# Optimization experiments

Hardware: AMD Instinct MI355X
Metric: run time of the kernel (lower is better)

The kernel has to match this reference:

```python
import jax, jax.numpy as jnp
import numpy as np

N, E, IN_DIM, HID, G, NCLS, LAYERS = 200000, 1200000, 128, 64, 1024, 6, 3
BN_EPS = 1e-5


def _bn(x, g, b, m, v):
    # eval-mode BatchNorm1d with running stats
    return (x - m) * jax.lax.rsqrt(v + BN_EPS) * g + b


def setup_inputs() -> dict:
    key = jax.random.key(0)
    ks = jax.random.split(key, 24)
    s = 0.05
    d = {
        "x": jax.random.normal(ks[0], (N, IN_DIM), jnp.float32),
        "edge_index": jax.random.randint(ks[1], (2, E), 0, N, dtype=jnp.int32),
        "batch": jnp.sort(jax.random.randint(ks[2], (N,), 0, G, dtype=jnp.int32)),
        # input embedding + input BN
        "emb_w": jax.random.normal(ks[3], (IN_DIM, HID), jnp.float32) * s,
        "emb_b": jnp.zeros((HID,), jnp.float32),
        "ibn_g": jnp.ones((HID,), jnp.float32),
        "ibn_b": jnp.zeros((HID,), jnp.float32),
        "ibn_m": jax.random.normal(ks[4], (HID,), jnp.float32) * 0.1,
        "ibn_v": jax.random.uniform(ks[5], (HID,), jnp.float32, 0.5, 1.5),
        # stacked per-layer GIN MLP params [LAYERS, ...]
        "fc1_w": jax.random.normal(ks[6], (LAYERS, HID, HID), jnp.float32) * s,
        "fc1_b": jnp.zeros((LAYERS, HID), jnp.float32),
        "mbn_g": jnp.ones((LAYERS, HID), jnp.float32),
        "mbn_b": jnp.zeros((LAYERS, HID), jnp.float32),
        "mbn_m": jax.random.normal(ks[7], (LAYERS, HID), jnp.float32) * 0.1,
        "mbn_v": jax.random.uniform(ks[8], (LAYERS, HID), jnp.float32, 0.5, 1.5),
        "fc2_w": jax.random.normal(ks[9], (LAYERS, HID, HID), jnp.float32) * s,
        "fc2_b": jnp.zeros((LAYERS, HID), jnp.float32),
        # stacked per-layer outer BN params
        "obn_g": jnp.ones((LAYERS, HID), jnp.float32),
        "obn_b": jnp.zeros((LAYERS, HID), jnp.float32),
        "obn_m": jax.random.normal(ks[10], (LAYERS, HID), jnp.float32) * 0.1,
        "obn_v": jax.random.uniform(ks[11], (LAYERS, HID), jnp.float32, 0.5, 1.5),
        # classifier head
        "cls1_w": jax.random.normal(ks[12], (HID, HID // 2), jnp.float32) * s,
        "cls1_b": jnp.zeros((HID // 2,), jnp.float32),
        "cls2_w": jax.random.normal(ks[13], (HID // 2, NCLS), jnp.float32) * s,
        "cls2_b": jnp.zeros((NCLS,), jnp.float32),
    }
    return d


def reference(x, edge_index, batch,
              emb_w, emb_b, ibn_g, ibn_b, ibn_m, ibn_v,
              fc1_w, fc1_b, mbn_g, mbn_b, mbn_m, mbn_v, fc2_w, fc2_b,
              obn_g, obn_b, obn_m, obn_v,
              cls1_w, cls1_b, cls2_w, cls2_b):
    n = x.shape[0]
    src, dst = edge_index[0], edge_index[1]

    # input embed -> BN -> relu (dropout = identity in eval)
    h = jnp.dot(x, emb_w) + emb_b
    h = jax.nn.relu(_bn(h, ibn_g, ibn_b, ibn_m, ibn_v))

    for i in range(LAYERS):
        # GINConv (eps=0): aggregate neighbors via scatter-add, then MLP
        agg = jax.ops.segment_sum(h[src], dst, num_segments=n)
        z = h + agg
        z = jnp.dot(z, fc1_w[i]) + fc1_b[i]
        z = jax.nn.relu(_bn(z, mbn_g[i], mbn_b[i], mbn_m[i], mbn_v[i]))
        z = jnp.dot(z, fc2_w[i]) + fc2_b[i]
        # outer BN + relu
        h = jax.nn.relu(_bn(z, obn_g[i], obn_b[i], obn_m[i], obn_v[i]))

    # global mean pool per graph
    sums = jax.ops.segment_sum(h, batch, num_segments=G)
    cnts = jax.ops.segment_sum(jnp.ones((n,), h.dtype), batch, num_segments=G)
    pooled = sums / jnp.maximum(cnts, 1.0)[:, None]

    # classifier
    out = jax.nn.relu(jnp.dot(pooled, cls1_w) + cls1_b)
    out = jnp.dot(out, cls2_w) + cls2_b
    return out
```

## Files before the change

kernel.cpp:

```cpp
#include <hip/hip_runtime.h>
#include <hip/hip_bf16.h>

#define N_NODES 200000
#define N_EDGES 1200000
#define IN_DIM  128
#define HID     64
#define NGRAPH  1024
#define NCLS    6
#define BN_EPS  1e-5f

#define TILE_N   64
#define ZS       68
#define ECAP     1024

#define NBKT   128
#define BRANGE 1568
#define BCAP   12288
#define EPB    4096
#define NB_BIN ((N_EDGES + EPB - 1) / EPB)

#define SWZ(s) ((s) ^ (((s) >> 4) & 3))

typedef short bf16x8 __attribute__((ext_vector_type(8)));
typedef float f32x4  __attribute__((ext_vector_type(4)));
#define MFMA16(a,b,c) __builtin_amdgcn_mfma_f32_16x16x32_bf16((a),(b),(c),0,0,0)

template<bool V> struct BoolC { static constexpr bool value = V; };

__device__ __forceinline__ unsigned short f2bf(float f) {
    union { __hip_bfloat16 h; unsigned short u; } v; v.h = __float2bfloat16(f); return v.u;
}
__device__ __forceinline__ float bfbits2f(unsigned short u) {
    union { unsigned int i; float f; } v; v.i = ((unsigned int)u) << 16; return v.f;
}
__device__ __forceinline__ void cvt4(const f32x4& x, uint2& hi, uint2& lo) {
    const unsigned short h0 = f2bf(x[0]), h1 = f2bf(x[1]), h2 = f2bf(x[2]), h3 = f2bf(x[3]);
    hi.x = (unsigned)h0 | ((unsigned)h1 << 16);
    hi.y = (unsigned)h2 | ((unsigned)h3 << 16);
    const unsigned short l0 = f2bf(x[0] - bfbits2f(h0)), l1 = f2bf(x[1] - bfbits2f(h1));
    const unsigned short l2 = f2bf(x[2] - bfbits2f(h2)), l3 = f2bf(x[3] - bfbits2f(h3));
    lo.x = (unsigned)l0 | ((unsigned)l1 << 16);
    lo.y = (unsigned)l2 | ((unsigned)l3 << 16);
}

__global__ __launch_bounds__(256) void setup_kernel(
    const float* __restrict__ emb_w, unsigned short* __restrict__ wpe,
    const float* __restrict__ fc1, const float* __restrict__ fc2,
    unsigned short* __restrict__ wpf,
    const int* __restrict__ batch, int* __restrict__ goffs,
    int* __restrict__ gcnt)
{
    const int b = blockIdx.x, t = threadIdx.x;
    if (b < 64) {
        const int idx = b * 256 + t;
        const int j = idx & 7, l = (idx >> 3) & 63;
        const int plane = (idx >> 9) & 1, s = (idx >> 10) & 3, ct = (idx >> 12) & 3;
        const int n = ct * 16 + (l & 15);
        const int k = s * 32 + (l >> 4) * 8 + j;
        const float f = emb_w[k * 64 + n];
        const unsigned short hb = f2bf(f);
        wpe[idx] = plane ? f2bf(f - bfbits2f(hb)) : hb;
    } else if (b < 256) {
        const int idx = (b - 64) * 256 + t;
        const int j = idx & 7, l = (idx >> 3) & 63;
        const int plane = (idx >> 9) & 1, s = (idx >> 10) & 1, ct = (idx >> 11) & 3;
        const int g = (idx >> 13) & 1, layer = idx >> 14;
        const int n = ct * 16 + (l & 15);
        const int k = s * 32 + (l >> 4) * 8 + j;
        const float* W = g ? fc2 : fc1;
        const float f = W[(layer * 64 + k) * 64 + n];
        const unsigned short hb = f2bf(f);
        wpf[idx] = plane ? f2bf(f - bfbits2f(hb)) : hb;
    } else {
        if (b == 256 && t < NBKT) gcnt[t] = 0;
        const int g = (b - 256) * 256 + t;
        if (g > NGRAPH) return;
        if (g == NGRAPH) { goffs[NGRAPH] = N_NODES; return; }
        int lo = 0, hi = N_NODES;
        while (lo < hi) {
            const int mid = (lo + hi) >> 1;
            if (batch[mid] < g) lo = mid + 1; else hi = mid;
        }
        goffs[g] = lo;
    }
}

__global__ __launch_bounds__(256) void bin_kernel(
    const int* __restrict__ src, const int* __restrict__ dst,
    int* __restrict__ gcnt, unsigned* __restrict__ ebin)
{
    __shared__ int hist[NBKT];
    __shared__ int basis[NBKT];
    const int t = threadIdx.x;
    const int base = blockIdx.x * EPB;
    if (t < NBKT) hist[t] = 0;
    __syncthreads();
    int sv[16], dv[16];
    #pragma unroll
    for (int i = 0; i < 16; i++) {
        const int e = base + t + i * 256;
        if (e < N_EDGES) {
            sv[i] = __builtin_nontemporal_load(&src[e]);
            dv[i] = __builtin_nontemporal_load(&dst[e]);
            atomicAdd(&hist[dv[i] / BRANGE], 1);
        } else { sv[i] = -1; dv[i] = -1; }
    }
    __syncthreads();
    if (t < NBKT) { basis[t] = atomicAdd(&gcnt[t], hist[t]); hist[t] = 0; }
    __syncthreads();
    #pragma unroll
    for (int i = 0; i < 16; i++) {
        if (dv[i] >= 0) {
            const int bb = dv[i] / BRANGE;
            const int dl = dv[i] - bb * BRANGE;
            const int pos = basis[bb] + atomicAdd(&hist[bb], 1);
            __builtin_nontemporal_store(
                (unsigned)sv[i] | ((unsigned)dl << 18),
                &ebin[(size_t)bb * BCAP + pos]);
        }
    }
}

__global__ __launch_bounds__(512) void binoffs_kernel(
    const int* __restrict__ gcnt, const unsigned* __restrict__ ebin,
    int* __restrict__ offs)
{
    __shared__ int hist[BRANGE];
    __shared__ int bscan[NBKT];
    __shared__ int pscan[512];
    const int b = blockIdx.x, t = threadIdx.x;
    for (int i = t; i < BRANGE; i += 512) hist[i] = 0;
    if (t < NBKT) bscan[t] = gcnt[t];
    __syncthreads();
    const int cnt = gcnt[b];
    const unsigned* __restrict__ eb = ebin + (size_t)b * BCAP;
    for (int i = t; i < cnt; i += 512) {
        const unsigned e = __builtin_nontemporal_load(&eb[i]);
        atomicAdd(&hist[e >> 18], 1);
    }
    __syncthreads();
    for (int off = 1; off < NBKT; off <<= 1) {
        const int u = (t >= off && t < NBKT) ? bscan[t - off] : 0;
        __syncthreads();
        if (t < NBKT) bscan[t] += u;
        __syncthreads();
    }
    const int bucketBase = (b == 0) ? 0 : bscan[b - 1];
    const int i0 = t * 4;
    const int h0v = (i0 + 0 < BRANGE) ? hist[i0 + 0] : 0;
    const int h1v = (i0 + 1 < BRANGE) ? hist[i0 + 1] : 0;
    const int h2v = (i0 + 2 < BRANGE) ? hist[i0 + 2] : 0;
    const int h3v = (i0 + 3 < BRANGE) ? hist[i0 + 3] : 0;
    const int ts = h0v + h1v + h2v + h3v;
    pscan[t] = ts;
    __syncthreads();
    for (int off = 1; off < 512; off <<= 1) {
        const int u = (t >= off) ? pscan[t - off] : 0;
        __syncthreads();
        pscan[t] += u;
        __syncthreads();
    }
    const int excl = pscan[t] - ts + bucketBase;
    const int r0 = b * BRANGE;
    if (i0 + 0 < BRANGE && r0 + i0 + 0 < N_NODES) offs[r0 + i0 + 0] = excl;
    if (i0 + 1 < BRANGE && r0 + i0 + 1 < N_NODES) offs[r0 + i0 + 1] = excl + h0v;
    if (i0 + 2 < BRANGE && r0 + i0 + 2 < N_NODES) offs[r0 + i0 + 2] = excl + h0v + h1v;
    if (i0 + 3 < BRANGE && r0 + i0 + 3 < N_NODES) offs[r0 + i0 + 3] = excl + h0v + h1v + h2v;
    if (b == NBKT - 1 && t == 0) offs[N_NODES] = N_EDGES;
}

__global__ __launch_bounds__(512) void binscatter_kernel(
    const int* __restrict__ gcnt, const unsigned* __restrict__ ebin,
    const int* __restrict__ offs, int* __restrict__ csr_src)
{
    __shared__ int cur[BRANGE];
    const int b = blockIdx.x, t = threadIdx.x;
    const int r0 = b * BRANGE;
    const int lim = (r0 + BRANGE <= N_NODES) ? BRANGE : (N_NODES - r0);
    for (int i = t; i < lim; i += 512) cur[i] = offs[r0 + i];
    __syncthreads();
    const int cnt = gcnt[b];
    const unsigned* __restrict__ eb = ebin + (size_t)b * BCAP;
    for (int i = t; i < cnt; i += 512) {
        const unsigned e = __builtin_nontemporal_load(&eb[i]);
        const int pos = atomicAdd(&cur[e >> 18], 1);
        csr_src[pos] = (int)(e & 0x3FFFFu);
    }
}

__global__ __launch_bounds__(256) void embed_kernel(
    const float* __restrict__ x, const unsigned short* __restrict__ wpe,
    const float* __restrict__ bias,
    const float* __restrict__ bn_g, const float* __restrict__ bn_b,
    const float* __restrict__ bn_m, const float* __restrict__ bn_v,
    float* __restrict__ h)
{
    __shared__ __align__(16) float Ush[8192];
    __shared__ float BNs[128];
    short* Abuf = (short*)Ush;
    float* Ztmp = Ush;
    const int t = threadIdx.x, lane = t & 63, w = t >> 6;
    const int base = blockIdx.x * TILE_N;

    if (t < 64) {
        const float s = bn_g[t] * rsqrtf(bn_v[t] + BN_EPS);
        BNs[t] = s;
        BNs[64 + t] = bias[t] * s + bn_b[t] - bn_m[t] * s;
    }
    #pragma unroll
    for (int i = 0; i < 8; i++) {
        const int idx = t + i * 256;
        const int n = idx >> 5, k4 = idx & 31;
        const f32x4 v = __builtin_nontemporal_load(
            (const f32x4*)(x + (size_t)(base + n) * IN_DIM + k4 * 4));
        uint2 hi, lo; cvt4(v, hi, lo);
        const int s = k4 >> 3, lc = (n & 15) + 16 * ((k4 >> 1) & 3);
        const int half = k4 & 1, wm = n >> 4;
        const int sl0 = ((wm * 4 + s) * 2 + 0) * 64 + lc;
        const int sl1 = ((wm * 4 + s) * 2 + 1) * 64 + lc;
        *(uint2*)&Abuf[SWZ(sl0) * 8 + half * 4] = hi;
        *(uint2*)&Abuf[SWZ(sl1) * 8 + half * 4] = lo;
    }
    __syncthreads();

    const bf16x8* A = (const bf16x8*)Abuf;
    const bf16x8* B = (const bf16x8*)wpe;
    bf16x8 ah[4], al[4];
    #pragma unroll
    for (int s = 0; s < 4; s++) {
        ah[s] = A[SWZ(((w * 4 + s) * 2 + 0) * 64 + lane)];
        al[s] = A[SWZ(((w * 4 + s) * 2 + 1) * 64 + lane)];
    }
    __syncthreads();
    const int q = lane >> 4, c = lane & 15;
    #pragma unroll
    for (int ct = 0; ct < 4; ct++) {
        f32x4 acc = {0.f, 0.f, 0.f, 0.f};
        #pragma unroll
        for (int s = 0; s < 4; s++) {
            const bf16x8 bh = B[(ct << 9) + (s << 7) + lane];
            const bf16x8 bl = B[(ct << 9) + (s << 7) + 64 + lane];
            acc = MFMA16(ah[s], bh, acc);
            acc = MFMA16(ah[s], bl, acc);
            acc = MFMA16(al[s], bh, acc);
        }
        const int n = ct * 16 + c;
        const float sc = BNs[n], sh = BNs[64 + n];
        #pragma unroll
        for (int r = 0; r < 4; r++)
            Ztmp[(w * 16 + q * 4 + r) * ZS + n] = fmaxf(acc[r] * sc + sh, 0.f);
    }
    __syncthreads();
    #pragma unroll
    for (int i = 0; i < 4; i++) {
        const int idx = t + i * 256, n = idx >> 4, k4 = idx & 15;
        *(f32x4*)(h + (size_t)(base + n) * HID + k4 * 4) =
            *(const f32x4*)(&Ztmp[n * ZS + k4 * 4]);
    }
}

template<bool POOL>
__global__ __launch_bounds__(256, 6) void agg_mlp_kernel(
    const float* __restrict__ hin, float* __restrict__ hout,
    const int* __restrict__ offs, const int* __restrict__ csr,
    const int* __restrict__ batch, float* __restrict__ pooled,
    const unsigned short* __restrict__ wp1, const unsigned short* __restrict__ wp2,
    const float* __restrict__ b1, const float* __restrict__ g1,
    const float* __restrict__ bb1, const float* __restrict__ m1, const float* __restrict__ v1,
    const float* __restrict__ b2, const float* __restrict__ g2,
    const float* __restrict__ bb2, const float* __restrict__ m2, const float* __restrict__ v2)
{
    __shared__ __align__(16) float Ush[TILE_N * ZS];
    __shared__ int   OF[TILE_N + 1];
    __shared__ int   EIDX[ECAP];
    __shared__ float BNs[256];
    __shared__ int   GID[TILE_N];
    short* Abuf = (short*)Ush;
    float* Ztmp = Ush;
    const int t = threadIdx.x, lane = t & 63, w = t >> 6;
    const int sub = lane >> 4, cq = lane & 15;
    const int base = blockIdx.x * TILE_N;

    if (t < 64) {
        const float sa = g1[t] * rsqrtf(v1[t] + BN_EPS);
        BNs[t] = sa; BNs[64 + t] = b1[t] * sa + bb1[t] - m1[t] * sa;
        const float sb = g2[t] * rsqrtf(v2[t] + BN_EPS);
        BNs[128 + t] = sb; BNs[192 + t] = b2[t] * sb + bb2[t] - m2[t] * sb;
        if (POOL) GID[t] = batch[base + t];
    }
    if (t <= TILE_N) OF[t] = offs[base + t];
    const int segStart = offs[base];
    const int segEnd   = offs[base + TILE_N];
    for (int i = t; i < segEnd - segStart; i += 256)
        if (i < ECAP) EIDX[i] = csr[segStart + i];
    __syncthreads();

    const float* __restrict__ hc = hin + cq * 4;
    const bool allLds = (segEnd - segStart) <= ECAP;

    auto gather_pass = [&](auto ldsTag) {
        constexpr bool LDSONLY = decltype(ldsTag)::value;
        #pragma unroll
        for (int pp = 0; pp < 2; pp++) {
            const int mlA = (pp * 2 + 0) * 4 + sub;
            const int mlB = (pp * 2 + 1) * 4 + sub;
            const int nlA = w * 16 + mlA, nlB = w * 16 + mlB;
            int eA = OF[nlA]; const int eA1 = OF[nlA + 1];
            int eB = OF[nlB]; const int eB1 = OF[nlB + 1];
            const int eAm = (eA1 - 1 > segStart) ? eA1 - 1 : segStart;
            const int eBm = (eB1 - 1 > segStart) ? eB1 - 1 : segStart;
            f32x4 accA = *(const f32x4*)(hin + (size_t)(base + nlA) * HID + cq * 4);
            f32x4 accB = *(const f32x4*)(hin + (size_t)(base + nlB) * HID + cq * 4);
            while (eA < eA1 || eB < eB1) {
                int ia[4], ib[4];
                #pragma unroll
                for (int k = 0; k < 4; k++) {
                    const int ea = (eA + k < eAm) ? eA + k : eAm;
                    const int eb = (eB + k < eBm) ? eB + k : eBm;
                    const int la = ea - segStart, lb = eb - segStart;
                    if (LDSONLY) {
                        ia[k] = EIDX[la];
                        ib[k] = EIDX[lb];
                    } else {
                        ia[k] = (la < ECAP) ? EIDX[la] : csr[ea];
                        ib[k] = (lb < ECAP) ? EIDX[lb] : csr[eb];
                    }
                }
                f32x4 va[4], vb[4];
                #pragma unroll
                for (int k = 0; k < 4; k++) {
                    va[k] = *(const f32x4*)(hc + (size_t)ia[k] * HID);
                    vb[k] = *(const f32x4*)(hc + (size_t)ib[k] * HID);
                }
                #pragma unroll
                for (int k = 0; k < 4; k++) {
                    const float ma = (eA + k < eA1) ? 1.f : 0.f;
                    const float mb = (eB + k < eB1) ? 1.f : 0.f;
                    accA += va[k] * ma;
                    accB += vb[k] * mb;
                }
                eA += 4; eB += 4;
            }
            {
                uint2 hi, lo; cvt4(accA, hi, lo);
                const int s = cq >> 3, lc = mlA + 16 * ((cq >> 1) & 3), half = cq & 1;
                const int sl0 = ((w * 2 + s) * 2 + 0) * 64 + lc;
                const int sl1 = ((w * 2 + s) * 2 + 1) * 64 + lc;
                *(uint2*)&Abuf[SWZ(sl0) * 8 + half * 4] = hi;
                *(uint2*)&Abuf[SWZ(sl1) * 8 + half * 4] = lo;
            }
            {
                uint2 hi, lo; cvt4(accB, hi, lo);
                const int s = cq >> 3, lc = mlB + 16 * ((cq >> 1) & 3), half = cq & 1;
                const int sl0 = ((w * 2 + s) * 2 + 0) * 64 + lc;
                const int sl1 = ((w * 2 + s) * 2 + 1) * 64 + lc;
                *(uint2*)&Abuf[SWZ(sl0) * 8 + half * 4] = hi;
                *(uint2*)&Abuf[SWZ(sl1) * 8 + half * 4] = lo;
            }
        }
    };
    if (allLds) gather_pass(BoolC<true>{});
    else        gather_pass(BoolC<false>{});
    __syncthreads();

    const bf16x8* A = (const bf16x8*)Abuf;
    const int q = lane >> 4, c = lane & 15;

    {
        const bf16x8 a0h = A[SWZ(((w * 2 + 0) * 2 + 0) * 64 + lane)];
        const bf16x8 a0l = A[SWZ(((w * 2 + 0) * 2 + 1) * 64 + lane)];
        const bf16x8 a1h = A[SWZ(((w * 2 + 1) * 2 + 0) * 64 + lane)];
        const bf16x8 a1l = A[SWZ(((w * 2 + 1) * 2 + 1) * 64 + lane)];
        __syncthreads();
        const bf16x8* B = (const bf16x8*)wp1;
        #pragma unroll
        for (int ct = 0; ct < 4; ct++) {
            const bf16x8 b0h = B[(ct << 8) + lane];
            const bf16x8 b0l = B[(ct << 8) + 64 + lane];
            const bf16x8 b1h_ = B[(ct << 8) + 128 + lane];
            const bf16x8 b1l_ = B[(ct << 8) + 192 + lane];
            f32x4 acc = {0.f, 0.f, 0.f, 0.f};
            acc = MFMA16(a0h, b0h, acc);
            acc = MFMA16(a0h, b0l, acc);
            acc = MFMA16(a0l, b0h, acc);
            acc = MFMA16(a1h, b1h_, acc);
            acc = MFMA16(a1h, b1l_, acc);
            acc = MFMA16(a1l, b1h_, acc);
            const int n = ct * 16 + c;
            const float sc = BNs[n], sh = BNs[64 + n];
            #pragma unroll
            for (int r = 0; r < 4; r++)
                Ztmp[(w * 16 + q * 4 + r) * ZS + n] = fmaxf(acc[r] * sc + sh, 0.f);
        }
    }
    __syncthreads();

    {
        const int m = t >> 2;
        f32x4 vv[4];
        #pragma unroll
        for (int d = 0; d < 4; d++) {
            const int k4 = (t & 3) * 4 + d;
            vv[d] = *(const f32x4*)(&Ztmp[m * ZS + k4 * 4]);
        }
        __syncthreads();
        #pragma unroll
        for (int d = 0; d < 4; d++) {
            const int k4 = (t & 3) * 4 + d;
            uint2 hi, lo; cvt4(vv[d], hi, lo);
            const int s = k4 >> 3, lc = (m & 15) + 16 * ((k4 >> 1) & 3);
            const int half = k4 & 1, wm = m >> 4;
            const int sl0 = ((wm * 2 + s) * 2 + 0) * 64 + lc;
            const int sl1 = ((wm * 2 + s) * 2 + 1) * 64 + lc;
            *(uint2*)&Abuf[SWZ(sl0) * 8 + half * 4] = hi;
            *(uint2*)&Abuf[SWZ(sl1) * 8 + half * 4] = lo;
        }
    }
    __syncthreads();

    {
        const bf16x8 a0h = A[SWZ(((w * 2 + 0) * 2 + 0) * 64 + lane)];
        const bf16x8 a0l = A[SWZ(((w * 2 + 0) * 2 + 1) * 64 + lane)];
        const bf16x8 a1h = A[SWZ(((w * 2 + 1) * 2 + 0) * 64 + lane)];
        const bf16x8 a1l = A[SWZ(((w * 2 + 1) * 2 + 1) * 64 + lane)];
        __syncthreads();
        const bf16x8* B = (const bf16x8*)wp2;
        #pragma unroll
        for (int ct = 0; ct < 4; ct++) {
            const bf16x8 b0h = B[(ct << 8) + lane];
            const bf16x8 b0l = B[(ct << 8) + 64 + lane];
            const bf16x8 b1h_ = B[(ct << 8) + 128 + lane];
            const bf16x8 b1l_ = B[(ct << 8) + 192 + lane];
            f32x4 acc = {0.f, 0.f, 0.f, 0.f};
            acc = MFMA16(a0h, b0h, acc);
            acc = MFMA16(a0h, b0l, acc);
            acc = MFMA16(a0l, b0h, acc);
            acc = MFMA16(a1h, b1h_, acc);
            acc = MFMA16(a1h, b1l_, acc);
            acc = MFMA16(a1l, b1h_, acc);
            const int n = ct * 16 + c;
            const float sc = BNs[128 + n], sh = BNs[192 + n];
            #pragma unroll
            for (int r = 0; r < 4; r++)
                Ztmp[(w * 16 + q * 4 + r) * ZS + n] = fmaxf(acc[r] * sc + sh, 0.f);
        }
    }
    __syncthreads();

    if (POOL) {
        const int cc = t & 63, rg = t >> 6;
        float run = 0.f;
        int cur = GID[rg * 16];
        #pragma unroll
        for (int r = 0; r < 16; r++) {
            const int row = rg * 16 + r;
            const int g = GID[row];
            if (g != cur) {
                atomicAdd(&pooled[(size_t)cur * HID + cc], run);
                run = 0.f; cur = g;
            }
            run += Ztmp[row * ZS + cc];
        }
        atomicAdd(&pooled[(size_t)cur * HID + cc], run);
    } else {
        #pragma unroll
        for (int i = 0; i < 4; i++) {
            const int idx = t + i * 256, n = idx >> 4, k4 = idx & 15;
            *(f32x4*)(hout + (size_t)(base + n) * HID + k4 * 4) =
                *(const f32x4*)(&Ztmp[n * ZS + k4 * 4]);
        }
    }
}

__global__ __launch_bounds__(64) void cls_kernel(
    const float* __restrict__ pooled, const int* __restrict__ goffs,
    const float* __restrict__ w1, const float* __restrict__ b1,
    const float* __restrict__ w2, const float* __restrict__ b2,
    float* __restrict__ out)
{
    const int g = blockIdx.x;
    const int lane = threadIdx.x;
    const float c = (float)(goffs[g + 1] - goffs[g]);
    const float p = pooled[(size_t)g * HID + lane] / fmaxf(c, 1.f);
    float acc = (lane < 32) ? b1[lane] : 0.f;
    #pragma unroll
    for (int k = 0; k < 64; k++) {
        const float pk = __shfl(p, k, 64);
        if (lane < 32) acc += pk * w1[k * 32 + lane];
    }
    const float hmid = fmaxf(acc, 0.f);
    float acc2 = (lane < NCLS) ? b2[lane] : 0.f;
    #pragma unroll
    for (int k = 0; k < 32; k++) {
        const float hk = __shfl(hmid, k, 64);
        if (lane < NCLS) acc2 += hk * w2[k * NCLS + lane];
    }
    if (lane < NCLS) out[(size_t)g * NCLS + lane] = acc2;
}

extern "C" void kernel_launch(void* const* d_in, const int* in_sizes, int n_in,
                              void* d_out, int out_size, void* d_ws, size_t ws_size,
                              hipStream_t stream) {
    const float* x     = (const float*)d_in[0];
    const int*   ei    = (const int*)d_in[1];
    const int*   batch = (const int*)d_in[2];
    const float* emb_w = (const float*)d_in[3];
    const float* emb_b = (const float*)d_in[4];
    const float* ibn_g = (const float*)d_in[5];
    const float* ibn_b = (const float*)d_in[6];
    const float* ibn_m = (const float*)d_in[7];
    const float* ibn_v = (const float*)d_in[8];
    const float* fc1_w = (const float*)d_in[9];
    const float* fc1_b = (const float*)d_in[10];
    const float* mbn_g = (const float*)d_in[11];
    const float* mbn_b = (const float*)d_in[12];
    const float* mbn_m = (const float*)d_in[13];
    const float* mbn_v = (const float*)d_in[14];
    const float* fc2_w = (const float*)d_in[15];
    const float* fc2_b = (const float*)d_in[16];
    const float* obn_g = (const float*)d_in[17];
    const float* obn_b = (const float*)d_in[18];
    const float* obn_m = (const float*)d_in[19];
    const float* obn_v = (const float*)d_in[20];
    const float* cls1w = (const float*)d_in[21];
    const float* cls1b = (const float*)d_in[22];
    const float* cls2w = (const float*)d_in[23];
    const float* cls2b = (const float*)d_in[24];

    float* h0     = (float*)d_ws;
    float* h1     = h0 + (size_t)N_NODES * HID;
    float* pooled = h1 + (size_t)N_NODES * HID;
    float* cnt    = pooled + NGRAPH * HID;
    int*   deg    = (int*)(cnt + NGRAPH);
    int*   offs   = deg + N_NODES;
    int*   bsum   = offs + (N_NODES + 1);
    int*   boff   = bsum + 256;
    int*   csr    = boff + 256;
    unsigned short* wpe = (unsigned short*)(csr + N_EDGES);
    unsigned short* wpf = wpe + 16384;
    int*   goffs  = (int*)(wpf + 49152);
    int*   gcnt   = goffs + (NGRAPH + 1);
    unsigned* ebin = (unsigned*)h0;

    const int* src = ei;
    const int* dst = ei + N_EDGES;

    setup_kernel<<<261, 256, 0, stream>>>(emb_w, wpe, fc1_w, fc2_w, wpf,
                                          batch, goffs, gcnt);
    hipMemsetAsync(pooled, 0, (size_t)NGRAPH * HID * sizeof(float), stream);

    bin_kernel<<<NB_BIN, 256, 0, stream>>>(src, dst, gcnt, ebin);
    binoffs_kernel<<<NBKT, 512, 0, stream>>>(gcnt, ebin, offs);
    binscatter_kernel<<<NBKT, 512, 0, stream>>>(gcnt, ebin, offs, csr);

    const int gemm_blocks = N_NODES / TILE_N;
    embed_kernel<<<gemm_blocks, 256, 0, stream>>>(x, wpe, emb_b,
                                                  ibn_g, ibn_b, ibn_m, ibn_v, h0);

    const float* hin = h0;
    float* hout = h1;
    for (int i = 0; i < 3; i++) {
        if (i < 2)
            agg_mlp_kernel<false><<<gemm_blocks, 256, 0, stream>>>(
                hin, hout, offs, csr, batch, pooled,
                wpf + (size_t)(i * 2 + 0) * 8192, wpf + (size_t)(i * 2 + 1) * 8192,
                fc1_b + i * HID, mbn_g + i * HID, mbn_b + i * HID, mbn_m + i * HID, mbn_v + i * HID,
                fc2_b + i * HID, obn_g + i * HID, obn_b + i * HID, obn_m + i * HID, obn_v + i * HID);
        else
            agg_mlp_kernel<true><<<gemm_blocks, 256, 0, stream>>>(
                hin, hout, offs, csr, batch, pooled,
                wpf + (size_t)(i * 2 + 0) * 8192, wpf + (size_t)(i * 2 + 1) * 8192,
                fc1_b + i * HID, mbn_g + i * HID, mbn_b + i * HID, mbn_m + i * HID, mbn_v + i * HID,
                fc2_b + i * HID, obn_g + i * HID, obn_b + i * HID, obn_m + i * HID, obn_v + i * HID);
        const float* tmp = hin; hin = hout; hout = (float*)tmp;
    }

    cls_kernel<<<NGRAPH, 64, 0, stream>>>(pooled, goffs, cls1w, cls1b, cls2w, cls2b,
                                          (float*)d_out);
}
```

Baseline: 465.7 us.

## Fuse edge binning into embed kernel and merge offset/scatter passes

Edge binning now runs as extra blocks of the embedding GEMM kernel, so the two independent jobs share one launch and can overlap. The bin buffer moves to h1 to avoid clobbering h0. The offset and scatter kernels are merged into one that stages each bucket's edges in shared memory, so the bucket is read from global memory once instead of twice. Zeroing of pooled moves into setup_kernel, replacing a memset. This cuts launches and global traffic, at the cost of more shared memory per block in the merged kernel (48KB bucket buffer plus histograms).

```diff
diff --git a/kernel.cpp b/kernel.cpp
--- a/kernel.cpp
+++ b/kernel.cpp
@@ -48,7 +48,7 @@
     const float* __restrict__ fc1, const float* __restrict__ fc2,
     unsigned short* __restrict__ wpf,
     const int* __restrict__ batch, int* __restrict__ goffs,
-    int* __restrict__ gcnt)
+    int* __restrict__ gcnt, float* __restrict__ pooled)
 {
     const int b = blockIdx.x, t = threadIdx.x;
     if (b < 64) {
@@ -71,7 +71,7 @@
         const float f = W[(layer * 64 + k) * 64 + n];
         const unsigned short hb = f2bf(f);
         wpf[idx] = plane ? f2bf(f - bfbits2f(hb)) : hb;
-    } else {
+    } else if (b < 261) {
         if (b == 256 && t < NBKT) gcnt[t] = 0;
         const int g = (b - 256) * 256 + t;
         if (g > NGRAPH) return;
@@ -82,113 +82,16 @@
             if (batch[mid] < g) lo = mid + 1; else hi = mid;
         }
         goffs[g] = lo;
-    }
-}
-
-__global__ __launch_bounds__(256) void bin_kernel(
+    } else {
+        const int idx = (b - 261) * 256 + t;
+        const f32x4 z = {0.f, 0.f, 0.f, 0.f};
+        *(f32x4*)(pooled + (size_t)idx * 4) = z;
+    }
+}
+
+__global__ __launch_bounds__(256) void csr_embed_kernel(
     const int* __restrict__ src, const int* __restrict__ dst,
-    int* __restrict__ gcnt, unsigned* __restrict__ ebin)
-{
-    __shared__ int hist[NBKT];
-    __shared__ int basis[NBKT];
-    const int t = threadIdx.x;
-    const int base = blockIdx.x * EPB;
-    if (t < NBKT) hist[t] = 0;
-    __syncthreads();
-    int sv[16], dv[16];
-    #pragma unroll
-    for (int i = 0; i < 16; i++) {
-        const int e = base + t + i * 256;
-        if (e < N_EDGES) {
-            sv[i] = __builtin_nontemporal_load(&src[e]);
-            dv[i] = __builtin_nontemporal_load(&dst[e]);
-            atomicAdd(&hist[dv[i] / BRANGE], 1);
-        } else { sv[i] = -1; dv[i] = -1; }
-    }
-    __syncthreads();
-    if (t < NBKT) { basis[t] = atomicAdd(&gcnt[t], hist[t]); hist[t] = 0; }
-    __syncthreads();
-    #pragma unroll
-    for (int i = 0; i < 16; i++) {
-        if (dv[i] >= 0) {
-            const int bb = dv[i] / BRANGE;
-            const int dl = dv[i] - bb * BRANGE;
-            const int pos = basis[bb] + atomicAdd(&hist[bb], 1);
-            __builtin_nontemporal_store(
-                (unsigned)sv[i] | ((unsigned)dl << 18),
-                &ebin[(size_t)bb * BCAP + pos]);
-        }
-    }
-}
-
-__global__ __launch_bounds__(512) void binoffs_kernel(
-    const int* __restrict__ gcnt, const unsigned* __restrict__ ebin,
-    int* __restrict__ offs)
-{
-    __shared__ int hist[BRANGE];
-    __shared__ int bscan[NBKT];
-    __shared__ int pscan[512];
-    const int b = blockIdx.x, t = threadIdx.x;
-    for (int i = t; i < BRANGE; i += 512) hist[i] = 0;
-    if (t < NBKT) bscan[t] = gcnt[t];
-    __syncthreads();
-    const int cnt = gcnt[b];
-    const unsigned* __restrict__ eb = ebin + (size_t)b * BCAP;
-    for (int i = t; i < cnt; i += 512) {
-        const unsigned e = __builtin_nontemporal_load(&eb[i]);
-        atomicAdd(&hist[e >> 18], 1);
-    }
-    __syncthreads();
-    for (int off = 1; off < NBKT; off <<= 1) {
-        const int u = (t >= off && t < NBKT) ? bscan[t - off] : 0;
-        __syncthreads();
-        if (t < NBKT) bscan[t] += u;
-        __syncthreads();
-    }
-    const int bucketBase = (b == 0) ? 0 : bscan[b - 1];
-    const int i0 = t * 4;
-    const int h0v = (i0 + 0 < BRANGE) ? hist[i0 + 0] : 0;
-    const int h1v = (i0 + 1 < BRANGE) ? hist[i0 + 1] : 0;
-    const int h2v = (i0 + 2 < BRANGE) ? hist[i0 + 2] : 0;
-    const int h3v = (i0 + 3 < BRANGE) ? hist[i0 + 3] : 0;
-    const int ts = h0v + h1v + h2v + h3v;
-    pscan[t] = ts;
-    __syncthreads();
-    for (int off = 1; off < 512; off <<= 1) {
-        const int u = (t >= off) ? pscan[t - off] : 0;
-        __syncthreads();
-        pscan[t] += u;
-        __syncthreads();
-    }
-    const int excl = pscan[t] - ts + bucketBase;
-    const int r0 = b * BRANGE;
-    if (i0 + 0 < BRANGE && r0 + i0 + 0 < N_NODES) offs[r0 + i0 + 0] = excl;
-    if (i0 + 1 < BRANGE && r0 + i0 + 1 < N_NODES) offs[r0 + i0 + 1] = excl + h0v;
-    if (i0 + 2 < BRANGE && r0 + i0 + 2 < N_NODES) offs[r0 + i0 + 2] = excl + h0v + h1v;
-    if (i0 + 3 < BRANGE && r0 + i0 + 3 < N_NODES) offs[r0 + i0 + 3] = excl + h0v + h1v + h2v;
-    if (b == NBKT - 1 && t == 0) offs[N_NODES] = N_EDGES;
-}
-
-__global__ __launch_bounds__(512) void binscatter_kernel(
-    const int* __restrict__ gcnt, const unsigned* __restrict__ ebin,
-    const int* __restrict__ offs, int* __restrict__ csr_src)
-{
-    __shared__ int cur[BRANGE];
-    const int b = blockIdx.x, t = threadIdx.x;
-    const int r0 = b * BRANGE;
-    const int lim = (r0 + BRANGE <= N_NODES) ? BRANGE : (N_NODES - r0);
-    for (int i = t; i < lim; i += 512) cur[i] = offs[r0 + i];
-    __syncthreads();
-    const int cnt = gcnt[b];
-    const unsigned* __restrict__ eb = ebin + (size_t)b * BCAP;
-    for (int i = t; i < cnt; i += 512) {
-        const unsigned e = __builtin_nontemporal_load(&eb[i]);
-        const int pos = atomicAdd(&cur[e >> 18], 1);
-        csr_src[pos] = (int)(e & 0x3FFFFu);
-    }
-}
-
-__global__ __launch_bounds__(256) void embed_kernel(
+    int* __restrict__ gcnt, unsigned* __restrict__ ebin,
     const float* __restrict__ x, const unsigned short* __restrict__ wpe,
     const float* __restrict__ bias,
     const float* __restrict__ bn_g, const float* __restrict__ bn_b,
@@ -197,10 +100,45 @@
 {
     __shared__ __align__(16) float Ush[8192];
     __shared__ float BNs[128];
+    const int t = threadIdx.x;
+
+    if (blockIdx.x < NB_BIN) {
+        int* hist  = (int*)Ush;
+        int* basis = hist + NBKT;
+        const int base = blockIdx.x * EPB;
+        if (t < NBKT) hist[t] = 0;
+        __syncthreads();
+        int sv[16], dv[16];
+        #pragma unroll
+        for (int i = 0; i < 16; i++) {
+            const int e = base + t + i * 256;
+            if (e < N_EDGES) {
+                sv[i] = __builtin_nontemporal_load(&src[e]);
+                dv[i] = __builtin_nontemporal_load(&dst[e]);
+                atomicAdd(&hist[dv[i] / BRANGE], 1);
+            } else { sv[i] = -1; dv[i] = -1; }
+        }
+        __syncthreads();
+        if (t < NBKT) { basis[t] = atomicAdd(&gcnt[t], hist[t]); hist[t] = 0; }
+        __syncthreads();
+        #pragma unroll
+        for (int i = 0; i < 16; i++) {
+            if (dv[i] >= 0) {
+                const int bb = dv[i] / BRANGE;
+                const int dl = dv[i] - bb * BRANGE;
+                const int pos = basis[bb] + atomicAdd(&hist[bb], 1);
+                __builtin_nontemporal_store(
+                    (unsigned)sv[i] | ((unsigned)dl << 18),
+                    &ebin[(size_t)bb * BCAP + pos]);
+            }
+        }
+        return;
+    }
+
     short* Abuf = (short*)Ush;
     float* Ztmp = Ush;
-    const int t = threadIdx.x, lane = t & 63, w = t >> 6;
-    const int base = blockIdx.x * TILE_N;
+    const int lane = t & 63, w = t >> 6;
+    const int base = (blockIdx.x - NB_BIN) * TILE_N;
 
     if (t < 64) {
         const float s = bn_g[t] * rsqrtf(bn_v[t] + BN_EPS);
@@ -256,6 +194,72 @@
         const int idx = t + i * 256, n = idx >> 4, k4 = idx & 15;
         *(f32x4*)(h + (size_t)(base + n) * HID + k4 * 4) =
             *(const f32x4*)(&Ztmp[n * ZS + k4 * 4]);
+    }
+}
+
+__global__ __launch_bounds__(512) void offs_scatter_kernel(
+    const int* __restrict__ gcnt, const unsigned* __restrict__ ebin,
+    int* __restrict__ offs, int* __restrict__ csr_src)
+{
+    __shared__ unsigned eb[BCAP];
+    __shared__ int hist[BRANGE];
+    __shared__ int bscan[NBKT];
+    __shared__ int pscan[512];
+    const int b = blockIdx.x, t = threadIdx.x;
+    const int cnt = gcnt[b];
+    for (int i = t; i < cnt; i += 512)
+        eb[i] = __builtin_nontemporal_load(&ebin[(size_t)b * BCAP + i]);
+    for (int i = t; i < BRANGE; i += 512) hist[i] = 0;
+    if (t < NBKT) bscan[t] = gcnt[t];
+    __syncthreads();
+    for (int i = t; i < cnt; i += 512)
+        atomicAdd(&hist[eb[i] >> 18], 1);
+    __syncthreads();
+    for (int off = 1; off < NBKT; off <<= 1) {
+        const int u = (t >= off && t < NBKT) ? bscan[t - off] : 0;
+        __syncthreads();
+        if (t < NBKT) bscan[t] += u;
+        __syncthreads();
+    }
+    const int bucketBase = (b == 0) ? 0 : bscan[b - 1];
+    const int i0 = t * 4;
+    const int h0v = (i0 + 0 < BRANGE) ? hist[i0 + 0] : 0;
+    const int h1v = (i0 + 1 < BRANGE) ? hist[i0 + 1] : 0;
+    const int h2v = (i0 + 2 < BRANGE) ? hist[i0 + 2] : 0;
+    const int h3v = (i0 + 3 < BRANGE) ? hist[i0 + 3] : 0;
+    const int ts = h0v + h1v + h2v + h3v;
+    pscan[t] = ts;
+    __syncthreads();
+    for (int off = 1; off < 512; off <<= 1) {
+        const int u = (t >= off) ? pscan[t - off] : 0;
+        __syncthreads();
+        pscan[t] += u;
+        __syncthreads();
+    }
+    const int excl = pscan[t] - ts + bucketBase;
+    const int r0 = b * BRANGE;
+    if (i0 + 0 < BRANGE) {
+        if (r0 + i0 + 0 < N_NODES) offs[r0 + i0 + 0] = excl;
+        hist[i0 + 0] = excl;
+    }
+    if (i0 + 1 < BRANGE) {
+        if (r0 + i0 + 1 < N_NODES) offs[r0 + i0 + 1] = excl + h0v;
+        hist[i0 + 1] = excl + h0v;
+    }
+    if (i0 + 2 < BRANGE) {
+        if (r0 + i0 + 2 < N_NODES) offs[r0 + i0 + 2] = excl + h0v + h1v;
+        hist[i0 + 2] = excl + h0v + h1v;
+    }
+    if (i0 + 3 < BRANGE) {
+        if (r0 + i0 + 3 < N_NODES) offs[r0 + i0 + 3] = excl + h0v + h1v + h2v;
+        hist[i0 + 3] = excl + h0v + h1v + h2v;
+    }
+    if (b == NBKT - 1 && t == 0) offs[N_NODES] = N_EDGES;
+    __syncthreads();
+    for (int i = t; i < cnt; i += 512) {
+        const unsigned e = eb[i];
+        const int pos = atomicAdd(&hist[e >> 18], 1);
+        csr_src[pos] = (int)(e & 0x3FFFFu);
     }
 }
 
@@ -540,22 +544,20 @@
     unsigned short* wpf = wpe + 16384;
     int*   goffs  = (int*)(wpf + 49152);
     int*   gcnt   = goffs + (NGRAPH + 1);
-    unsigned* ebin = (unsigned*)h0;
+    unsigned* ebin = (unsigned*)h1;
 
     const int* src = ei;
     const int* dst = ei + N_EDGES;
 
-    setup_kernel<<<261, 256, 0, stream>>>(emb_w, wpe, fc1_w, fc2_w, wpf,
-                                          batch, goffs, gcnt);
-    hipMemsetAsync(pooled, 0, (size_t)NGRAPH * HID * sizeof(float), stream);
-
-    bin_kernel<<<NB_BIN, 256, 0, stream>>>(src, dst, gcnt, ebin);
-    binoffs_kernel<<<NBKT, 512, 0, stream>>>(gcnt, ebin, offs);
-    binscatter_kernel<<<NBKT, 512, 0, stream>>>(gcnt, ebin, offs, csr);
+    setup_kernel<<<325, 256, 0, stream>>>(emb_w, wpe, fc1_w, fc2_w, wpf,
+                                          batch, goffs, gcnt, pooled);
 
     const int gemm_blocks = N_NODES / TILE_N;
-    embed_kernel<<<gemm_blocks, 256, 0, stream>>>(x, wpe, emb_b,
-                                                  ibn_g, ibn_b, ibn_m, ibn_v, h0);
+    csr_embed_kernel<<<NB_BIN + gemm_blocks, 256, 0, stream>>>(
+        src, dst, gcnt, ebin,
+        x, wpe, emb_b, ibn_g, ibn_b, ibn_m, ibn_v, h0);
+
+    offs_scatter_kernel<<<NBKT, 512, 0, stream>>>(gcnt, ebin, offs, csr);
 
     const float* hin = h0;
     float* hout = h1;
```

After: 463.6 us. About the same (-0.5%).
